# Kernel tuning notes

Measured on AMD Instinct MI355X. Metric: run time of the kernel, lower is better.

The kernel has to match this reference:

```python
import jax, jax.numpy as jnp
import numpy as np


def _max_pairwise_dist(l, r):
    # l: [N, d], r: [M, d]
    # squared distances via Gram trick: ||l||^2 + ||r||^2 - 2 l.r  -> [N, M]
    l_sq = jnp.sum(l * l, axis=-1)  # [N]
    r_sq = jnp.sum(r * r, axis=-1)  # [M]
    cross = jnp.einsum('nd,md->nm', l, r)  # [N, M]
    sq_dists = l_sq[:, None] + r_sq[None, :] - 2.0 * cross
    sq_dists = jnp.maximum(sq_dists, 0.0)  # guard tiny negatives
    return jnp.sqrt(jnp.max(sq_dists))  # sqrt of max == max of sqrt (monotone)


def setup_inputs() -> dict:
    key = jax.random.key(0)
    k1, k2 = jax.random.split(key)
    N, M, D = 8192, 8192, 64
    return {
        'l_dfa_embeddings': jax.random.normal(k1, (N, D), dtype=jnp.float32),
        'r_dfa_embeddings': jax.random.normal(k2, (M, D), dtype=jnp.float32),
    }


def reference(l_dfa_embeddings, r_dfa_embeddings):
    # Max over all pairwise L2 distances between l and r state embeddings
    return _max_pairwise_dist(l_dfa_embeddings, r_dfa_embeddings)
```

## Files before the change

### kernel.cpp

```cpp
#include <hip/hip_runtime.h>
#include <hip/hip_bf16.h>
#include <math.h>


typedef __attribute__((ext_vector_type(8)))  short  short8;
typedef __attribute__((ext_vector_type(4)))  float  f32x4;
typedef __attribute__((ext_vector_type(16))) float  f32x16;

constexpr int D  = 64;
constexpr int NR = 8192;

__device__ __forceinline__ short f2bf(float f) {
    __hip_bfloat16 h = __float2bfloat16(f);
    return __builtin_bit_cast(short, h);
}


__global__ __launch_bounds__(256) void prepack_kernel(
    const float* __restrict__ L, const float* __restrict__ R,
    short* __restrict__ Apk, short* __restrict__ Bpk,
    float* __restrict__ lsq, float* __restrict__ rsq,
    unsigned int* __restrict__ outbits)
{
    const int t = blockIdx.x * 256 + threadIdx.x;
    const int r = t >> 3;
    const int j = t & 7;
    const int kk = j >> 1, kh = j & 1;
    const bool isL = (r < NR);
    const int rr = isL ? r : r - NR;

    const float* src = (isL ? L : R) + (size_t)rr * D + j * 8;
    short* pk = isL ? Apk : Bpk;

    f32x4 v0 = *reinterpret_cast<const f32x4*>(src + 0);
    f32x4 v1 = *reinterpret_cast<const f32x4*>(src + 4);

    float p = 0.f;
    #pragma unroll
    for (int e = 0; e < 4; ++e) { p = fmaf(v0[e], v0[e], p); p = fmaf(v1[e], v1[e], p); }

    short8 w;
    #pragma unroll
    for (int e = 0; e < 4; ++e) { w[e] = f2bf(v0[e]); w[4+e] = f2bf(v1[e]); }
    *reinterpret_cast<short8*>(
        pk + ((size_t)(rr >> 5) * 4 + kk) * 512 + (kh * 32 + (rr & 31)) * 8) = w;

    p += __shfl_xor(p, 1, 64);
    p += __shfl_xor(p, 2, 64);
    p += __shfl_xor(p, 4, 64);
    if (j == 0) (isL ? lsq : rsq)[rr] = p;

    if (t == 0) *outbits = 0u;
}

__global__ __launch_bounds__(256, 2) void pairdist_mfma_kernel(
    const short* __restrict__ Apk, const short* __restrict__ Bpk,
    const float* __restrict__ lsq, const float* __restrict__ rsq,
    unsigned int* __restrict__ outbits)
{
    __shared__ __align__(16) short A_lds[16][4][64][8];

    const int tid  = threadIdx.x;
    const int lane = tid & 63;
    const int wave = tid >> 6;
    const int xc = blockIdx.x;
    const int yb = blockIdx.y;

    {
        const short* At = Apk + (size_t)(xc * 16) * 2048;
        short* Al = &A_lds[0][0][0][0];
        #pragma unroll
        for (int i = 0; i < 16; ++i) {
            const int off = (i * 4 + wave) * 512;
            __builtin_amdgcn_global_load_lds(
                (const __attribute__((address_space(1))) unsigned int*)(At + off + lane * 8),
                (__attribute__((address_space(3))) unsigned int*)(Al + off),
                16, 0, 0);
        }
    }

    const int wm = wave >> 1;
    const int wn = wave & 1;
    short8 bf[4][4];
    #pragma unroll
    for (int nj = 0; nj < 4; ++nj)
        #pragma unroll
        for (int kk = 0; kk < 4; ++kk)
            bf[nj][kk] = *reinterpret_cast<const short8*>(
                Bpk + ((size_t)(yb * 8 + wn * 4 + nj) * 4 + kk) * 512 + lane * 8);

    const int col = lane & 31;
    const int h   = lane >> 5;
    float rq[4];
    #pragma unroll
    for (int nj = 0; nj < 4; ++nj)
        rq[nj] = rsq[yb * 256 + wn * 128 + nj * 32 + col];

    __syncthreads();

    float lmax = 0.f;
    #pragma unroll
    for (int t = 0; t < 4; ++t) {
        f32x4 lqv[2][4];
        #pragma unroll
        for (int mi = 0; mi < 2; ++mi) {
            const int rbase = xc * 512 + t * 128 + (wm * 2 + mi) * 32 + 4 * h;
            #pragma unroll
            for (int g = 0; g < 4; ++g)
                lqv[mi][g] = *reinterpret_cast<const f32x4*>(lsq + rbase + g * 8);
        }

        f32x16 acc[2][4] = {};
        #pragma unroll
        for (int kk = 0; kk < 4; ++kk) {
            short8 a0 = *reinterpret_cast<const short8*>(&A_lds[t*4 + wm*2 + 0][kk][lane][0]);
            short8 a1 = *reinterpret_cast<const short8*>(&A_lds[t*4 + wm*2 + 1][kk][lane][0]);
            acc[0][0] = __builtin_amdgcn_mfma_f32_32x32x16_bf16(a0, bf[0][kk], acc[0][0], 0, 0, 0);
            acc[0][1] = __builtin_amdgcn_mfma_f32_32x32x16_bf16(a0, bf[1][kk], acc[0][1], 0, 0, 0);
            acc[0][2] = __builtin_amdgcn_mfma_f32_32x32x16_bf16(a0, bf[2][kk], acc[0][2], 0, 0, 0);
            acc[0][3] = __builtin_amdgcn_mfma_f32_32x32x16_bf16(a0, bf[3][kk], acc[0][3], 0, 0, 0);
            acc[1][0] = __builtin_amdgcn_mfma_f32_32x32x16_bf16(a1, bf[0][kk], acc[1][0], 0, 0, 0);
            acc[1][1] = __builtin_amdgcn_mfma_f32_32x32x16_bf16(a1, bf[1][kk], acc[1][1], 0, 0, 0);
            acc[1][2] = __builtin_amdgcn_mfma_f32_32x32x16_bf16(a1, bf[2][kk], acc[1][2], 0, 0, 0);
            acc[1][3] = __builtin_amdgcn_mfma_f32_32x32x16_bf16(a1, bf[3][kk], acc[1][3], 0, 0, 0);
        }

        #pragma unroll
        for (int mi = 0; mi < 2; ++mi) {
            #pragma unroll
            for (int nj = 0; nj < 4; ++nj) {
                float x[16];
                #pragma unroll
                for (int g = 0; g < 4; ++g)
                    #pragma unroll
                    for (int e = 0; e < 4; ++e)
                        x[g*4+e] = fmaf(-2.f, acc[mi][nj][g*4 + e], lqv[mi][g][e]);
                float y0 = fmaxf(x[0],  x[1]),  y1 = fmaxf(x[2],  x[3]);
                float y2 = fmaxf(x[4],  x[5]),  y3 = fmaxf(x[6],  x[7]);
                float y4 = fmaxf(x[8],  x[9]),  y5 = fmaxf(x[10], x[11]);
                float y6 = fmaxf(x[12], x[13]), y7 = fmaxf(x[14], x[15]);
                float z0 = fmaxf(y0, y1), z1 = fmaxf(y2, y3);
                float z2 = fmaxf(y4, y5), z3 = fmaxf(y6, y7);
                float m  = fmaxf(fmaxf(z0, z1), fmaxf(z2, z3));
                lmax = fmaxf(lmax, m + rq[nj]);
            }
        }
    }

    #pragma unroll
    for (int off = 32; off >= 1; off >>= 1)
        lmax = fmaxf(lmax, __shfl_xor(lmax, off, 64));

    __syncthreads();
    float* wmax = reinterpret_cast<float*>(&A_lds[0][0][0][0]);
    if (lane == 0) wmax[wave] = lmax;
    __syncthreads();
    if (tid == 0) {
        float bmax = fmaxf(fmaxf(wmax[0], wmax[1]), fmaxf(wmax[2], wmax[3]));
        bmax = sqrtf(fmaxf(bmax, 0.f));
        atomicMax(outbits, __float_as_uint(bmax));
    }
}

extern "C" void kernel_launch(void* const* d_in, const int* in_sizes, int n_in,
                              void* d_out, int out_size, void* d_ws, size_t ws_size,
                              hipStream_t stream) {
    const float* L = (const float*)d_in[0];
    const float* R = (const float*)d_in[1];

    short* Apk = (short*)d_ws;
    short* Bpk = Apk + (size_t)NR * D;
    float* lsqg = (float*)(Bpk + (size_t)NR * D);
    float* rsqg = lsqg + NR;
    unsigned int* outbits = (unsigned int*)d_out;

    prepack_kernel<<<(2 * NR * 8) / 256, 256, 0, stream>>>(L, R, Apk, Bpk, lsqg, rsqg, outbits);
    pairdist_mfma_kernel<<<dim3(16, 32), dim3(256), 0, stream>>>(Apk, Bpk, lsqg, rsqg, outbits);
}
```

Measured before the change: 23.27 us.

## Shrink per-block tile to 128x128 and launch 4096 blocks for more parallelism

The pairwise kernel's block tile shrinks from 512x256 to 128x128, and the grid becomes a flat 4096-block launch with higher launch-bounds occupancy. LDS per block drops and the t-loop goes away, so there are many more, smaller blocks to fill the 256 CUs and hide latency. In exchange, B fragments, the rsq/lsq loads and the per-block atomicMax are repeated across many more blocks, so there is more global traffic and more atomic contention.

```diff
diff --git a/kernel.cpp b/kernel.cpp
--- a/kernel.cpp
+++ b/kernel.cpp
@@ -53,110 +53,99 @@
     if (t == 0) *outbits = 0u;
 }
 
-__global__ __launch_bounds__(256, 2) void pairdist_mfma_kernel(
+__global__ __launch_bounds__(256, 4) void pairdist_mfma_kernel(
     const short* __restrict__ Apk, const short* __restrict__ Bpk,
     const float* __restrict__ lsq, const float* __restrict__ rsq,
     unsigned int* __restrict__ outbits)
 {
-    __shared__ __align__(16) short A_lds[16][4][64][8];
+    __shared__ __align__(16) short A_lds[4][4][64][8];
+    __shared__ float wmax_s[4];
 
     const int tid  = threadIdx.x;
     const int lane = tid & 63;
     const int wave = tid >> 6;
-    const int xc = blockIdx.x;
-    const int yb = blockIdx.y;
+    const int bid  = blockIdx.x;
+    const int xc = bid & 63;
+    const int yb = bid >> 6;
 
     {
-        const short* At = Apk + (size_t)(xc * 16) * 2048;
-        short* Al = &A_lds[0][0][0][0];
+        const short* At = Apk + (size_t)(xc * 4) * 2048;
         #pragma unroll
-        for (int i = 0; i < 16; ++i) {
-            const int off = (i * 4 + wave) * 512;
+        for (int i = 0; i < 4; ++i)
             __builtin_amdgcn_global_load_lds(
-                (const __attribute__((address_space(1))) unsigned int*)(At + off + lane * 8),
-                (__attribute__((address_space(3))) unsigned int*)(Al + off),
+                (const __attribute__((address_space(1))) unsigned int*)
+                    (At + ((size_t)i * 4 + wave) * 512 + lane * 8),
+                (__attribute__((address_space(3))) unsigned int*)
+                    (&A_lds[i][wave][0][0]),
                 16, 0, 0);
-        }
     }
 
     const int wm = wave >> 1;
     const int wn = wave & 1;
-    short8 bf[4][4];
+    short8 bf[2][4];
     #pragma unroll
-    for (int nj = 0; nj < 4; ++nj)
+    for (int nj = 0; nj < 2; ++nj)
         #pragma unroll
         for (int kk = 0; kk < 4; ++kk)
             bf[nj][kk] = *reinterpret_cast<const short8*>(
-                Bpk + ((size_t)(yb * 8 + wn * 4 + nj) * 4 + kk) * 512 + lane * 8);
+                Bpk + ((size_t)(yb * 4 + wn * 2 + nj) * 4 + kk) * 512 + lane * 8);
 
     const int col = lane & 31;
     const int h   = lane >> 5;
-    float rq[4];
+    float rq[2];
     #pragma unroll
-    for (int nj = 0; nj < 4; ++nj)
-        rq[nj] = rsq[yb * 256 + wn * 128 + nj * 32 + col];
+    for (int nj = 0; nj < 2; ++nj)
+        rq[nj] = rsq[yb * 128 + (wn * 2 + nj) * 32 + col];
 
     __syncthreads();
 
+    f32x16 acc[2][2] = {};
+    #pragma unroll
+    for (int kk = 0; kk < 4; ++kk) {
+        short8 a0 = *reinterpret_cast<const short8*>(&A_lds[wm*2 + 0][kk][lane][0]);
+        short8 a1 = *reinterpret_cast<const short8*>(&A_lds[wm*2 + 1][kk][lane][0]);
+        acc[0][0] = __builtin_amdgcn_mfma_f32_32x32x16_bf16(a0, bf[0][kk], acc[0][0], 0, 0, 0);
+        acc[0][1] = __builtin_amdgcn_mfma_f32_32x32x16_bf16(a0, bf[1][kk], acc[0][1], 0, 0, 0);
+        acc[1][0] = __builtin_amdgcn_mfma_f32_32x32x16_bf16(a1, bf[0][kk], acc[1][0], 0, 0, 0);
+        acc[1][1] = __builtin_amdgcn_mfma_f32_32x32x16_bf16(a1, bf[1][kk], acc[1][1], 0, 0, 0);
+    }
+
     float lmax = 0.f;
     #pragma unroll
-    for (int t = 0; t < 4; ++t) {
-        f32x4 lqv[2][4];
+    for (int mi = 0; mi < 2; ++mi) {
+        const int rbase = xc * 128 + (wm * 2 + mi) * 32 + 4 * h;
+        f32x4 lq0 = *reinterpret_cast<const f32x4*>(lsq + rbase +  0);
+        f32x4 lq1 = *reinterpret_cast<const f32x4*>(lsq + rbase +  8);
+        f32x4 lq2 = *reinterpret_cast<const f32x4*>(lsq + rbase + 16);
+        f32x4 lq3 = *reinterpret_cast<const f32x4*>(lsq + rbase + 24);
         #pragma unroll
-        for (int mi = 0; mi < 2; ++mi) {
-            const int rbase = xc * 512 + t * 128 + (wm * 2 + mi) * 32 + 4 * h;
+        for (int nj = 0; nj < 2; ++nj) {
+            float x[16];
             #pragma unroll
-            for (int g = 0; g < 4; ++g)
-                lqv[mi][g] = *reinterpret_cast<const f32x4*>(lsq + rbase + g * 8);
-        }
-
-        f32x16 acc[2][4] = {};
-        #pragma unroll
-        for (int kk = 0; kk < 4; ++kk) {
-            short8 a0 = *reinterpret_cast<const short8*>(&A_lds[t*4 + wm*2 + 0][kk][lane][0]);
-            short8 a1 = *reinterpret_cast<const short8*>(&A_lds[t*4 + wm*2 + 1][kk][lane][0]);
-            acc[0][0] = __builtin_amdgcn_mfma_f32_32x32x16_bf16(a0, bf[0][kk], acc[0][0], 0, 0, 0);
-            acc[0][1] = __builtin_amdgcn_mfma_f32_32x32x16_bf16(a0, bf[1][kk], acc[0][1], 0, 0, 0);
-            acc[0][2] = __builtin_amdgcn_mfma_f32_32x32x16_bf16(a0, bf[2][kk], acc[0][2], 0, 0, 0);
-            acc[0][3] = __builtin_amdgcn_mfma_f32_32x32x16_bf16(a0, bf[3][kk], acc[0][3], 0, 0, 0);
-            acc[1][0] = __builtin_amdgcn_mfma_f32_32x32x16_bf16(a1, bf[0][kk], acc[1][0], 0, 0, 0);
-            acc[1][1] = __builtin_amdgcn_mfma_f32_32x32x16_bf16(a1, bf[1][kk], acc[1][1], 0, 0, 0);
-            acc[1][2] = __builtin_amdgcn_mfma_f32_32x32x16_bf16(a1, bf[2][kk], acc[1][2], 0, 0, 0);
-            acc[1][3] = __builtin_amdgcn_mfma_f32_32x32x16_bf16(a1, bf[3][kk], acc[1][3], 0, 0, 0);
-        }
-
-        #pragma unroll
-        for (int mi = 0; mi < 2; ++mi) {
-            #pragma unroll
-            for (int nj = 0; nj < 4; ++nj) {
-                float x[16];
-                #pragma unroll
-                for (int g = 0; g < 4; ++g)
-                    #pragma unroll
-                    for (int e = 0; e < 4; ++e)
-                        x[g*4+e] = fmaf(-2.f, acc[mi][nj][g*4 + e], lqv[mi][g][e]);
-                float y0 = fmaxf(x[0],  x[1]),  y1 = fmaxf(x[2],  x[3]);
-                float y2 = fmaxf(x[4],  x[5]),  y3 = fmaxf(x[6],  x[7]);
-                float y4 = fmaxf(x[8],  x[9]),  y5 = fmaxf(x[10], x[11]);
-                float y6 = fmaxf(x[12], x[13]), y7 = fmaxf(x[14], x[15]);
-                float z0 = fmaxf(y0, y1), z1 = fmaxf(y2, y3);
-                float z2 = fmaxf(y4, y5), z3 = fmaxf(y6, y7);
-                float m  = fmaxf(fmaxf(z0, z1), fmaxf(z2, z3));
-                lmax = fmaxf(lmax, m + rq[nj]);
+            for (int e = 0; e < 4; ++e) {
+                x[0  + e] = fmaf(-2.f, acc[mi][nj][0  + e], lq0[e]);
+                x[4  + e] = fmaf(-2.f, acc[mi][nj][4  + e], lq1[e]);
+                x[8  + e] = fmaf(-2.f, acc[mi][nj][8  + e], lq2[e]);
+                x[12 + e] = fmaf(-2.f, acc[mi][nj][12 + e], lq3[e]);
             }
+            float y0 = fmaxf(x[0],  x[1]),  y1 = fmaxf(x[2],  x[3]);
+            float y2 = fmaxf(x[4],  x[5]),  y3 = fmaxf(x[6],  x[7]);
+            float y4 = fmaxf(x[8],  x[9]),  y5 = fmaxf(x[10], x[11]);
+            float y6 = fmaxf(x[12], x[13]), y7 = fmaxf(x[14], x[15]);
+            float z0 = fmaxf(y0, y1), z1 = fmaxf(y2, y3);
+            float z2 = fmaxf(y4, y5), z3 = fmaxf(y6, y7);
+            float m  = fmaxf(fmaxf(z0, z1), fmaxf(z2, z3));
+            lmax = fmaxf(lmax, m + rq[nj]);
         }
     }
 
     #pragma unroll
     for (int off = 32; off >= 1; off >>= 1)
         lmax = fmaxf(lmax, __shfl_xor(lmax, off, 64));
-
-    __syncthreads();
-    float* wmax = reinterpret_cast<float*>(&A_lds[0][0][0][0]);
-    if (lane == 0) wmax[wave] = lmax;
+    if (lane == 0) wmax_s[wave] = lmax;
     __syncthreads();
     if (tid == 0) {
-        float bmax = fmaxf(fmaxf(wmax[0], wmax[1]), fmaxf(wmax[2], wmax[3]));
+        float bmax = fmaxf(fmaxf(wmax_s[0], wmax_s[1]), fmaxf(wmax_s[2], wmax_s[3]));
         bmax = sqrtf(fmaxf(bmax, 0.f));
         atomicMax(outbits, __float_as_uint(bmax));
     }
@@ -175,5 +164,5 @@
     unsigned int* outbits = (unsigned int*)d_out;
 
     prepack_kernel<<<(2 * NR * 8) / 256, 256, 0, stream>>>(L, R, Apk, Bpk, lsqg, rsqg, outbits);
-    pairdist_mfma_kernel<<<dim3(16, 32), dim3(256), 0, stream>>>(Apk, Bpk, lsqg, rsqg, outbits);
+    pairdist_mfma_kernel<<<4096, 256, 0, stream>>>(Apk, Bpk, lsqg, rsqg, outbits);
 }
```

Result: slower. 60.36 us (+159.4%).
